# Optimization experiments

Hardware: AMD Instinct MI355X
Metric: run time of the kernel (lower is better)

## Reference

```python
import jax, jax.numpy as jnp
import numpy as np
from jax import lax

B, P, C = 2, 512, 5                 # images, proposals/img, classes (incl. background)
IN_FEAT, REP = 12544, 1024          # 256*7*7 pooled features; TwoMLPHead width
H_IMG = W_IMG = 800.0
SCORE_THRESH, NMS_THRESH, DET_PER_IMG = 0.05, 0.5, 100
MIN_SIZE = 0.01
WX, WY, WW, WH = 10.0, 10.0, 5.0, 5.0
BBOX_CLIP = float(np.log(1000.0 / 16.0))
NEG = -1e9


def _make_boxes(key, n):
    k1, k2, k3, k4 = jax.random.split(key, 4)
    cx = jax.random.uniform(k1, (n,)) * W_IMG
    cy = jax.random.uniform(k2, (n,)) * H_IMG
    bw = jax.random.uniform(k3, (n,)) * 180.0 + 20.0
    bh = jax.random.uniform(k4, (n,)) * 180.0 + 20.0
    x1 = jnp.clip(cx - bw / 2, 0.0, W_IMG)
    y1 = jnp.clip(cy - bh / 2, 0.0, H_IMG)
    x2 = jnp.clip(cx + bw / 2, 0.0, W_IMG)
    y2 = jnp.clip(cy + bh / 2, 0.0, H_IMG)
    return jnp.stack([x1, y1, x2, y2], -1).astype(jnp.float32)


def setup_inputs() -> dict:
    ks = jax.random.split(jax.random.key(0), 12)
    box_features = jax.random.normal(ks[0], (B * P, IN_FEAT), jnp.float32)
    proposals = jnp.stack([_make_boxes(ks[1 + i], P) for i in range(B)])
    def w(k, shp):
        return (jax.random.normal(k, shp, jnp.float32) / np.sqrt(shp[0])).astype(jnp.float32)
    return {
        'box_features': box_features,
        'proposals': proposals,
        'W1': w(ks[3], (IN_FEAT, REP)), 'b1': jnp.zeros((REP,), jnp.float32),
        'W2': w(ks[4], (REP, REP)),     'b2': jnp.zeros((REP,), jnp.float32),
        'Wc': w(ks[5], (REP, C)),       'bc': jnp.zeros((C,), jnp.float32),
        'Wb': w(ks[6], (REP, 4 * C)),   'bb': jnp.zeros((4 * C,), jnp.float32),
    }


def box_iou(a, b):
    area_a = (a[:, 2] - a[:, 0]) * (a[:, 3] - a[:, 1])
    area_b = (b[:, 2] - b[:, 0]) * (b[:, 3] - b[:, 1])
    lt = jnp.maximum(a[:, None, :2], b[None, :, :2])
    rb = jnp.minimum(a[:, None, 2:], b[None, :, 2:])
    wh = jnp.clip(rb - lt, 0.0)
    inter = wh[..., 0] * wh[..., 1]
    return inter / (area_a[:, None] + area_b[None, :] - inter + 1e-9)


def decode(reg, props):
    # reg: [N, C, 4] raw deltas; props: [N, 4] xyxy  (torchvision BoxCoder.decode)
    w = props[:, 2] - props[:, 0]
    h = props[:, 3] - props[:, 1]
    cx = props[:, 0] + 0.5 * w
    cy = props[:, 1] + 0.5 * h
    dx, dy = reg[..., 0] / WX, reg[..., 1] / WY
    dw = jnp.minimum(reg[..., 2] / WW, BBOX_CLIP)
    dh = jnp.minimum(reg[..., 3] / WH, BBOX_CLIP)
    pcx = dx * w[:, None] + cx[:, None]
    pcy = dy * h[:, None] + cy[:, None]
    pw = jnp.exp(dw) * w[:, None]
    ph = jnp.exp(dh) * h[:, None]
    return jnp.stack([pcx - 0.5 * pw, pcy - 0.5 * ph, pcx + 0.5 * pw, pcy + 0.5 * ph], -1)


def postprocess_one(boxes, scores, labels):
    # boxes [M,4] (already clipped), scores [M], labels [M] int; fixed-size output.
    M = boxes.shape[0]
    ws = boxes[:, 2] - boxes[:, 0]
    hs = boxes[:, 3] - boxes[:, 1]
    valid = (scores > SCORE_THRESH) & (ws >= MIN_SIZE) & (hs >= MIN_SIZE)
    order = jnp.argsort(-scores)
    b, s, l, v = boxes[order], scores[order], labels[order], valid[order]
    # batched (per-class) NMS via class-offset trick
    off = l.astype(b.dtype)[:, None] * (max(H_IMG, W_IMG) + 1.0)
    iou = box_iou(b + off, b + off)
    idxs = jnp.arange(M)

    def body(i, keep):
        sup = (iou[i] > NMS_THRESH) & keep[i] & (idxs > i)
        return keep & ~sup

    keep = lax.fori_loop(0, M, body, v)
    sc = jnp.where(keep, s, NEG)
    top_s, top_i = lax.top_k(sc, DET_PER_IMG)
    ok = top_s > NEG / 2
    tb = jnp.where(ok[:, None], b[top_i], 0.0)
    tl = jnp.where(ok, l[top_i], 0)
    ts = jnp.where(ok, top_s, 0.0)
    return tb, ts, tl


def reference(box_features, proposals, W1, b1, W2, b2, Wc, bc, Wb, bb):
    # box_head: TwoMLPHead
    h = jax.nn.relu(box_features @ W1 + b1)
    h = jax.nn.relu(h @ W2 + b2)
    # box_predictor
    class_logits = h @ Wc + bc                       # [N, C]
    box_regression = (h @ Wb + bb).reshape(-1, C, 4)  # [N, C, 4]
    props = proposals.reshape(-1, 4)
    pred = decode(box_regression, props)             # [N, C, 4]
    # clip to image
    pred = jnp.stack([
        jnp.clip(pred[..., 0], 0.0, W_IMG), jnp.clip(pred[..., 1], 0.0, H_IMG),
        jnp.clip(pred[..., 2], 0.0, W_IMG), jnp.clip(pred[..., 3], 0.0, H_IMG)], -1)
    scores = jax.nn.softmax(class_logits, -1)        # [N, C]
    # drop background class, flatten proposal-major (matches torch reshape(-1,4))
    pb = pred[:, 1:, :].reshape(B, P * (C - 1), 4)
    sc = scores[:, 1:].reshape(B, P * (C - 1))
    labels = jnp.tile(jnp.arange(1, C, dtype=jnp.int32), P)  # [M]
    boxes_o, scores_o, labels_o = jax.vmap(postprocess_one, in_axes=(0, 0, None))(pb, sc, labels)
    return boxes_o, scores_o, labels_o
```

## Files before the change

### kernel.cpp

```cpp
#include <hip/hip_runtime.h>
#include <math.h>

#define NROWS 1024
#define K1    12544
#define REP   1024
#define NDET  2048
#define DETS  100
#define BBOX_CLIP_F 4.135166556742356f

typedef __attribute__((ext_vector_type(8))) short bf16x8;
typedef __attribute__((ext_vector_type(4))) float f32x4;

__device__ __forceinline__ unsigned short rne_bf16(float x) {
  unsigned u = __float_as_uint(x);
  u += 0x7fffu + ((u >> 16) & 1u);
  return (unsigned short)(u >> 16);
}
__device__ __forceinline__ float bf16f(unsigned short h) {
  return __uint_as_float(((unsigned)h) << 16);
}
__device__ __forceinline__ int swz(int r, int s) {
  return s ^ (r & 3) ^ ((r >> 2) & 3);
}
__device__ __forceinline__ void gload16(const void* g, void* lds) {
  __builtin_amdgcn_global_load_lds(
      (const __attribute__((address_space(1))) unsigned int*)g,
      (__attribute__((address_space(3))) unsigned int*)lds, 16, 0, 0);
}

__global__ __launch_bounds__(256) void pack_b(
    const float* __restrict__ W, unsigned short* __restrict__ Oh,
    unsigned short* __restrict__ Ol, int nKB) {
  __shared__ unsigned short th[32 * 36], tl[32 * 36];
  const int kb = blockIdx.x, n0 = blockIdx.y * 32;
  const int t = threadIdx.x;
  const int r = t >> 3, c4 = (t & 7) << 2;
  float4 v = *(const float4*)&W[(size_t)(kb * 32 + r) * REP + n0 + c4];
  float fv[4] = {v.x, v.y, v.z, v.w};
#pragma unroll
  for (int j = 0; j < 4; ++j) {
    unsigned short h = rne_bf16(fv[j]);
    th[(c4 + j) * 36 + r] = h;
    tl[(c4 + j) * 36 + r] = rne_bf16(fv[j] - bf16f(h));
  }
  __syncthreads();
  const int half = t >> 7;
  const int n_loc = (t & 127) >> 2, slot = t & 3;
  const unsigned short* src = (half ? tl : th) + n_loc * 36 + slot * 8;
  ushort4 u0 = *(const ushort4*)src;
  ushort4 u1 = *(const ushort4*)(src + 4);
  const int n = n0 + n_loc, rb = n >> 7, rr = n & 127;
  size_t chunk = ((size_t)(rb * nKB + kb)) * 512 + rr * 4 + swz(rr, slot);
  unsigned short* dst = (half ? Ol : Oh) + chunk * 8;
  *(ushort4*)dst = u0;
  *(ushort4*)(dst + 4) = u1;
}

__global__ __launch_bounds__(256) void pack_a(
    const float* __restrict__ A, unsigned short* __restrict__ Oh,
    unsigned short* __restrict__ Ol, int K, int nKB) {
  const int kb = blockIdx.x;
  const int r = blockIdx.y * 64 + (threadIdx.x >> 2);
  const int slot = threadIdx.x & 3;
  const float* p = A + (size_t)r * K + kb * 32 + slot * 8;
  float4 f0 = *(const float4*)p;
  float4 f1 = *(const float4*)(p + 4);
  float fv[8] = {f0.x, f0.y, f0.z, f0.w, f1.x, f1.y, f1.z, f1.w};
  unsigned short hh[8], ll[8];
#pragma unroll
  for (int j = 0; j < 8; ++j) {
    hh[j] = rne_bf16(fv[j]);
    ll[j] = rne_bf16(fv[j] - bf16f(hh[j]));
  }
  const int rb = r >> 7, rr = r & 127;
  size_t chunk = ((size_t)(rb * nKB + kb)) * 512 + rr * 4 + swz(rr, slot);
  unsigned short* dh = Oh + chunk * 8;
  unsigned short* dl = Ol + chunk * 8;
  *(ushort4*)dh = make_ushort4(hh[0], hh[1], hh[2], hh[3]);
  *(ushort4*)(dh + 4) = make_ushort4(hh[4], hh[5], hh[6], hh[7]);
  *(ushort4*)dl = make_ushort4(ll[0], ll[1], ll[2], ll[3]);
  *(ushort4*)(dl + 4) = make_ushort4(ll[4], ll[5], ll[6], ll[7]);
}

__global__ __launch_bounds__(256) void gemm_pk2(
    const unsigned short* __restrict__ Ah, const unsigned short* __restrict__ Al,
    const unsigned short* __restrict__ Bh, const unsigned short* __restrict__ Bl,
    float* __restrict__ T, int nKB, int stepsPerZ) {
  __shared__ __align__(16) unsigned short lds[2][4][4096];
  const int tid = threadIdx.x;
  const int w = tid >> 6, l = tid & 63;
  const int r_ = blockIdx.x, t_ = blockIdx.y;
  const int rbA = (r_ & 3) * 2 + (t_ & 1);
  const int rbB = (r_ >> 2) * 4 + (t_ >> 1);
  const int tk0 = blockIdx.z * stepsPerZ;
  const int fr = l & 15, q = l >> 4;
  const int wr = (w >> 1) * 64, wc = (w & 1) * 64;
  const int qs = q ^ (fr & 3) ^ (fr >> 2);
  const int aoff = ((wr + fr) * 4 + qs) * 16;
  const int boff = ((wc + fr) * 4 + qs) * 16;

  auto stage = [&](int bf, int tk) {
    const unsigned short* ga_h = Ah + ((size_t)(rbA * nKB + tk)) * 4096;
    const unsigned short* ga_l = Al + ((size_t)(rbA * nKB + tk)) * 4096;
    const unsigned short* gb_h = Bh + ((size_t)(rbB * nKB + tk)) * 4096;
    const unsigned short* gb_l = Bl + ((size_t)(rbB * nKB + tk)) * 4096;
#pragma unroll
    for (int rseg = 0; rseg < 2; ++rseg) {
      const int seg = rseg * 4 + w;
      const size_t go = (size_t)(seg * 64 + l) * 8;
      gload16(ga_h + go, &lds[bf][0][seg * 512]);
      gload16(ga_l + go, &lds[bf][1][seg * 512]);
      gload16(gb_h + go, &lds[bf][2][seg * 512]);
      gload16(gb_l + go, &lds[bf][3][seg * 512]);
    }
  };

  f32x4 acc[4][4];
#pragma unroll
  for (int m = 0; m < 4; ++m)
#pragma unroll
    for (int n = 0; n < 4; ++n) acc[m][n] = (f32x4){0.f, 0.f, 0.f, 0.f};

  stage(0, tk0);
  __syncthreads();
  int cur = 0;
  for (int s = 0; s < stepsPerZ; ++s) {
    if (s + 1 < stepsPerZ) stage(cur ^ 1, tk0 + s + 1);
    const char* La  = (const char*)&lds[cur][0][0];
    const char* Ll  = (const char*)&lds[cur][1][0];
    const char* Lbh = (const char*)&lds[cur][2][0];
    const char* Lbl = (const char*)&lds[cur][3][0];
    bf16x8 ah[4], al[4], bh[4], bl[4];
#pragma unroll
    for (int m = 0; m < 4; ++m) {
      ah[m] = *(const bf16x8*)(La + aoff + m * 1024);
      al[m] = *(const bf16x8*)(Ll + aoff + m * 1024);
    }
#pragma unroll
    for (int n = 0; n < 4; ++n) {
      bh[n] = *(const bf16x8*)(Lbh + boff + n * 1024);
      bl[n] = *(const bf16x8*)(Lbl + boff + n * 1024);
    }
#pragma unroll
    for (int m = 0; m < 4; ++m)
#pragma unroll
      for (int n = 0; n < 4; ++n) {
        acc[m][n] = __builtin_amdgcn_mfma_f32_16x16x32_bf16(ah[m], bh[n], acc[m][n], 0, 0, 0);
        acc[m][n] = __builtin_amdgcn_mfma_f32_16x16x32_bf16(ah[m], bl[n], acc[m][n], 0, 0, 0);
        acc[m][n] = __builtin_amdgcn_mfma_f32_16x16x32_bf16(al[m], bh[n], acc[m][n], 0, 0, 0);
      }
    __syncthreads();
    cur ^= 1;
  }
  float* Tz = T + (size_t)blockIdx.z * (NROWS * REP);
#pragma unroll
  for (int m = 0; m < 4; ++m) {
    const int r0 = rbA * 128 + wr + m * 16 + ((l >> 4) << 2);
#pragma unroll
    for (int n = 0; n < 4; ++n) {
      const int c = rbB * 128 + wc + n * 16 + fr;
#pragma unroll
      for (int j = 0; j < 4; ++j) Tz[(size_t)(r0 + j) * REP + c] = acc[m][n][j];
    }
  }
}

__global__ __launch_bounds__(256) void combine8_relu_pack(
    const float* __restrict__ T, const float* __restrict__ bias,
    unsigned short* __restrict__ Oh, unsigned short* __restrict__ Ol) {
  const int e = (blockIdx.x * 256 + threadIdx.x) * 8;
  const int MN = NROWS * REP;
  float s[8];
  {
    float4 a0 = *(const float4*)&T[e];
    float4 a1 = *(const float4*)&T[e + 4];
    s[0] = a0.x; s[1] = a0.y; s[2] = a0.z; s[3] = a0.w;
    s[4] = a1.x; s[5] = a1.y; s[6] = a1.z; s[7] = a1.w;
  }
#pragma unroll
  for (int z = 1; z < 8; ++z) {
    float4 a0 = *(const float4*)&T[z * MN + e];
    float4 a1 = *(const float4*)&T[z * MN + e + 4];
    s[0] += a0.x; s[1] += a0.y; s[2] += a0.z; s[3] += a0.w;
    s[4] += a1.x; s[5] += a1.y; s[6] += a1.z; s[7] += a1.w;
  }
  const int c0 = e & 1023;
  float4 b0 = *(const float4*)&bias[c0];
  float4 b1 = *(const float4*)&bias[c0 + 4];
  s[0] = fmaxf(s[0] + b0.x, 0.f); s[1] = fmaxf(s[1] + b0.y, 0.f);
  s[2] = fmaxf(s[2] + b0.z, 0.f); s[3] = fmaxf(s[3] + b0.w, 0.f);
  s[4] = fmaxf(s[4] + b1.x, 0.f); s[5] = fmaxf(s[5] + b1.y, 0.f);
  s[6] = fmaxf(s[6] + b1.z, 0.f); s[7] = fmaxf(s[7] + b1.w, 0.f);
  unsigned short hh[8], ll[8];
#pragma unroll
  for (int j = 0; j < 8; ++j) {
    hh[j] = rne_bf16(s[j]);
    ll[j] = rne_bf16(s[j] - bf16f(hh[j]));
  }
  const int r = e >> 10;
  const int kb = c0 >> 5, slot = (c0 >> 3) & 3;
  const int rb = r >> 7, rr = r & 127;
  size_t chunk = ((size_t)(rb * 32 + kb)) * 512 + rr * 4 + swz(rr, slot);
  unsigned short* dh = Oh + chunk * 8;
  unsigned short* dl = Ol + chunk * 8;
  *(ushort4*)dh = make_ushort4(hh[0], hh[1], hh[2], hh[3]);
  *(ushort4*)(dh + 4) = make_ushort4(hh[4], hh[5], hh[6], hh[7]);
  *(ushort4*)dl = make_ushort4(ll[0], ll[1], ll[2], ll[3]);
  *(ushort4*)(dl + 4) = make_ushort4(ll[4], ll[5], ll[6], ll[7]);
}

__global__ __launch_bounds__(256) void combine8_relu(
    const float* __restrict__ T, const float* __restrict__ bias, float* __restrict__ H) {
  const int i = blockIdx.x * 256 + threadIdx.x;
  const int MN4 = NROWS * REP / 4;
  const float4* t = (const float4*)T;
  float4 s0 = t[i];
#pragma unroll
  for (int z = 1; z < 8; ++z) {
    float4 v = t[i + z * MN4];
    s0.x += v.x; s0.y += v.y; s0.z += v.z; s0.w += v.w;
  }
  float4 bs = ((const float4*)bias)[i & 255];
  float4 r;
  r.x = fmaxf(s0.x + bs.x, 0.f);
  r.y = fmaxf(s0.y + bs.y, 0.f);
  r.z = fmaxf(s0.z + bs.z, 0.f);
  r.w = fmaxf(s0.w + bs.w, 0.f);
  ((float4*)H)[i] = r;
}

__global__ __launch_bounds__(256) void gemm_pk(
    const float* __restrict__ A, const unsigned short* __restrict__ Bh,
    const unsigned short* __restrict__ Bl, float* __restrict__ T,
    int K, int nKB, int stepsPerZ) {
  __shared__ __align__(16) unsigned short lds[2][4][4096];
  const int tid = threadIdx.x;
  const int w = tid >> 6, l = tid & 63;
  const int bm = blockIdx.x * 128;
  const int bnb = blockIdx.y;
  const int tk0 = blockIdx.z * stepsPerZ;
  const int arow = tid >> 1, ahalf = tid & 1;
  const int fr = l & 15, q = l >> 4;
  const int wr = (w >> 1) * 64, wc = (w & 1) * 64;
  const int qs = q ^ (fr & 3) ^ (fr >> 2);
  const int aoff = ((wr + fr) * 4 + qs) * 16;
  const int boff = ((wc + fr) * 4 + qs) * 16;
  const float* aptr = A + (size_t)(bm + arow) * K + ahalf * 16;

  float4 av[4];
  auto loadA = [&](int tk) {
    const float* p = aptr + tk * 32;
#pragma unroll
    for (int j = 0; j < 4; ++j) av[j] = *(const float4*)(p + j * 4);
  };
  auto stageB = [&](int bf, int tk) {
    const unsigned short* gh = Bh + ((size_t)(bnb * nKB + tk)) * 4096;
    const unsigned short* gl_ = Bl + ((size_t)(bnb * nKB + tk)) * 4096;
#pragma unroll
    for (int rseg = 0; rseg < 2; ++rseg) {
      const int seg = rseg * 4 + w;
      gload16(gh + (size_t)(seg * 64 + l) * 8, &lds[bf][2][seg * 512]);
      gload16(gl_ + (size_t)(seg * 64 + l) * 8, &lds[bf][3][seg * 512]);
    }
  };
  auto writeA = [&](int bf) {
#pragma unroll
    for (int j = 0; j < 2; ++j) {
      const int s_ = ahalf * 2 + j;
      float fv[8] = {av[j * 2].x, av[j * 2].y, av[j * 2].z, av[j * 2].w,
                     av[j * 2 + 1].x, av[j * 2 + 1].y, av[j * 2 + 1].z, av[j * 2 + 1].w};
      unsigned hp[4], lp[4];
#pragma unroll
      for (int p2 = 0; p2 < 4; ++p2) {
        unsigned short h0 = rne_bf16(fv[2 * p2]), h1 = rne_bf16(fv[2 * p2 + 1]);
        float l0 = fv[2 * p2] - bf16f(h0), l1 = fv[2 * p2 + 1] - bf16f(h1);
        hp[p2] = (unsigned)h0 | ((unsigned)h1 << 16);
        lp[p2] = (unsigned)rne_bf16(l0) | ((unsigned)rne_bf16(l1) << 16);
      }
      const int chunk = arow * 4 + swz(arow, s_);
      *(uint4*)&lds[bf][0][chunk * 8] = make_uint4(hp[0], hp[1], hp[2], hp[3]);
      *(uint4*)&lds[bf][1][chunk * 8] = make_uint4(lp[0], lp[1], lp[2], lp[3]);
    }
  };

  f32x4 acc[4][4];
#pragma unroll
  for (int m = 0; m < 4; ++m)
#pragma unroll
    for (int n = 0; n < 4; ++n) acc[m][n] = (f32x4){0.f, 0.f, 0.f, 0.f};

  loadA(tk0);
  stageB(0, tk0);
  writeA(0);
  __syncthreads();
  int cur = 0;
  for (int s = 0; s < stepsPerZ; ++s) {
    const bool nx = (s + 1 < stepsPerZ);
    if (nx) { loadA(tk0 + s + 1); stageB(cur ^ 1, tk0 + s + 1); }
    const char* La = (const char*)&lds[cur][0][0];
    const char* Ll = (const char*)&lds[cur][1][0];
    const char* Lbh = (const char*)&lds[cur][2][0];
    const char* Lbl = (const char*)&lds[cur][3][0];
    bf16x8 ah[4], al[4], bh[4], bl[4];
#pragma unroll
    for (int m = 0; m < 4; ++m) {
      ah[m] = *(const bf16x8*)(La + aoff + m * 1024);
      al[m] = *(const bf16x8*)(Ll + aoff + m * 1024);
    }
#pragma unroll
    for (int n = 0; n < 4; ++n) {
      bh[n] = *(const bf16x8*)(Lbh + boff + n * 1024);
      bl[n] = *(const bf16x8*)(Lbl + boff + n * 1024);
    }
#pragma unroll
    for (int m = 0; m < 4; ++m)
#pragma unroll
      for (int n = 0; n < 4; ++n) {
        acc[m][n] = __builtin_amdgcn_mfma_f32_16x16x32_bf16(ah[m], bh[n], acc[m][n], 0, 0, 0);
        acc[m][n] = __builtin_amdgcn_mfma_f32_16x16x32_bf16(ah[m], bl[n], acc[m][n], 0, 0, 0);
        acc[m][n] = __builtin_amdgcn_mfma_f32_16x16x32_bf16(al[m], bh[n], acc[m][n], 0, 0, 0);
      }
    if (nx) writeA(cur ^ 1);
    __syncthreads();
    cur ^= 1;
  }
  float* Tz = T + (size_t)blockIdx.z * (NROWS * REP);
#pragma unroll
  for (int m = 0; m < 4; ++m) {
    const int r0 = bm + wr + m * 16 + ((l >> 4) << 2);
#pragma unroll
    for (int n = 0; n < 4; ++n) {
      const int c = bnb * 128 + wc + n * 16 + fr;
#pragma unroll
      for (int j = 0; j < 4; ++j) Tz[(size_t)(r0 + j) * REP + c] = acc[m][n][j];
    }
  }
}

__global__ __launch_bounds__(256) void gemm64(
    const float* __restrict__ A, const float* __restrict__ W,
    float* __restrict__ T, int K, int N, int kChunk) {
  __shared__ float As[32][68];
  __shared__ float Bs[32][64];
  const int tid = threadIdx.x;
  const int bm = blockIdx.x * 64, bn = blockIdx.y * 64;
  const int k0 = blockIdx.z * kChunk;
  const int tx = tid & 15, ty = tid >> 4;
  const int ar = tid >> 3;
  const int ac = (tid & 7) << 2;
  const int br = tid >> 4;
  const int bc = (tid & 15) << 2;
  float acc[4][4] = {{0.f,0.f,0.f,0.f},{0.f,0.f,0.f,0.f},{0.f,0.f,0.f,0.f},{0.f,0.f,0.f,0.f}};
  for (int kk = k0; kk < k0 + kChunk; kk += 32) {
    float4 a0 = *(const float4*)&A[(size_t)(bm + ar) * K + kk + ac];
    float4 a1 = *(const float4*)&A[(size_t)(bm + ar + 32) * K + kk + ac];
    float4 b0 = *(const float4*)&W[(size_t)(kk + br) * N + bn + bc];
    float4 b1 = *(const float4*)&W[(size_t)(kk + br + 16) * N + bn + bc];
    As[ac+0][ar] = a0.x; As[ac+1][ar] = a0.y; As[ac+2][ar] = a0.z; As[ac+3][ar] = a0.w;
    As[ac+0][ar+32] = a1.x; As[ac+1][ar+32] = a1.y; As[ac+2][ar+32] = a1.z; As[ac+3][ar+32] = a1.w;
    *(float4*)&Bs[br][bc]    = b0;
    *(float4*)&Bs[br+16][bc] = b1;
    __syncthreads();
#pragma unroll
    for (int k = 0; k < 32; ++k) {
      float4 av = *(const float4*)&As[k][ty << 2];
      float4 bv = *(const float4*)&Bs[k][tx << 2];
      float a_[4] = {av.x, av.y, av.z, av.w};
      float b_[4] = {bv.x, bv.y, bv.z, bv.w};
#pragma unroll
      for (int i = 0; i < 4; ++i)
#pragma unroll
        for (int j = 0; j < 4; ++j)
          acc[i][j] = fmaf(a_[i], b_[j], acc[i][j]);
    }
    __syncthreads();
  }
  float* Tz = T + (size_t)blockIdx.z * NROWS * REP;
#pragma unroll
  for (int i = 0; i < 4; ++i) {
    float4 v = make_float4(acc[i][0], acc[i][1], acc[i][2], acc[i][3]);
    *(float4*)&Tz[(size_t)(bm + (ty << 2) + i) * N + bn + (tx << 2)] = v;
  }
}

__global__ __launch_bounds__(256) void combine_relu(
    const float* __restrict__ T, const float* __restrict__ bias, float* __restrict__ H) {
  const int i = blockIdx.x * 256 + threadIdx.x;
  const int MN4 = NROWS * REP / 4;
  const float4* t = (const float4*)T;
  float4 a = t[i], b = t[i + MN4], c = t[i + 2 * MN4], d = t[i + 3 * MN4];
  float4 bs = ((const float4*)bias)[i & 255];
  float4 r;
  r.x = fmaxf(((a.x + b.x) + (c.x + d.x)) + bs.x, 0.f);
  r.y = fmaxf(((a.y + b.y) + (c.y + d.y)) + bs.y, 0.f);
  r.z = fmaxf(((a.z + b.z) + (c.z + d.z)) + bs.z, 0.f);
  r.w = fmaxf(((a.w + b.w) + (c.w + d.w)) + bs.w, 0.f);
  ((float4*)H)[i] = r;
}

__global__ __launch_bounds__(256) void pack_w25(
    const float* __restrict__ Wc, const float* __restrict__ Wb, float* __restrict__ Wt) {
  const int i = blockIdx.x * 256 + threadIdx.x;
  if (i < 25 * 1024) {
    const int o = i >> 10, k = i & 1023;
    Wt[i] = (o < 5) ? Wc[(size_t)k * 5 + o] : Wb[(size_t)k * 20 + (o - 5)];
  }
}

__global__ __launch_bounds__(256) void heads2(
    const float* __restrict__ H2, const float* __restrict__ Wt,
    const float* __restrict__ bcv, const float* __restrict__ bbv,
    const float* __restrict__ props, float* __restrict__ pb, float* __restrict__ sc) {
  const int wave = threadIdx.x >> 6, l = threadIdx.x & 63;
  const int n = blockIdx.x * 4 + wave;
  const float* h = H2 + (size_t)n * REP + l * 16;
  float4 h0 = *(const float4*)h, h1 = *(const float4*)(h + 4);
  float4 h2v = *(const float4*)(h + 8), h3 = *(const float4*)(h + 12);
  float outv[25];
#pragma unroll
  for (int o = 0; o < 25; ++o) {
    const float* wp = Wt + o * REP + l * 16;
    float4 w0 = *(const float4*)wp, w1 = *(const float4*)(wp + 4);
    float4 w2 = *(const float4*)(wp + 8), w3 = *(const float4*)(wp + 12);
    float d = h0.x * w0.x;
    d = fmaf(h0.y, w0.y, d); d = fmaf(h0.z, w0.z, d); d = fmaf(h0.w, w0.w, d);
    d = fmaf(h1.x, w1.x, d); d = fmaf(h1.y, w1.y, d); d = fmaf(h1.z, w1.z, d); d = fmaf(h1.w, w1.w, d);
    d = fmaf(h2v.x, w2.x, d); d = fmaf(h2v.y, w2.y, d); d = fmaf(h2v.z, w2.z, d); d = fmaf(h2v.w, w2.w, d);
    d = fmaf(h3.x, w3.x, d); d = fmaf(h3.y, w3.y, d); d = fmaf(h3.z, w3.z, d); d = fmaf(h3.w, w3.w, d);
#pragma unroll
    for (int m = 1; m < 64; m <<= 1) d += __shfl_xor(d, m);
    outv[o] = d + ((o < 5) ? bcv[o] : bbv[o - 5]);
  }
  const float mx = fmaxf(fmaxf(fmaxf(outv[0], outv[1]), fmaxf(outv[2], outv[3])), outv[4]);
  const float e0 = expf(outv[0] - mx), e1 = expf(outv[1] - mx), e2 = expf(outv[2] - mx);
  const float e3 = expf(outv[3] - mx), e4 = expf(outv[4] - mx);
  const float inv = 1.0f / (e0 + e1 + e2 + e3 + e4);
  const float s1 = e1 * inv, s2 = e2 * inv, s3 = e3 * inv, s4 = e4 * inv;
  const float* pr = props + (size_t)n * 4;
  const float x1 = pr[0], y1 = pr[1], x2 = pr[2], y2 = pr[3];
  const float bw = x2 - x1, bh = y2 - y1;
  const float cx = x1 + 0.5f * bw, cy = y1 + 0.5f * bh;
  const int img = n >> 9, pbase = (n & 511) << 2;
#pragma unroll
  for (int c = 1; c <= 4; ++c) {
    if (l == c - 1) {
      const float r0 = outv[5 + c * 4 + 0], r1 = outv[5 + c * 4 + 1];
      const float r2 = outv[5 + c * 4 + 2], r3 = outv[5 + c * 4 + 3];
      const float dx = r0 / 10.0f, dy = r1 / 10.0f;
      const float dw = fminf(r2 / 5.0f, BBOX_CLIP_F);
      const float dh = fminf(r3 / 5.0f, BBOX_CLIP_F);
      const float pcx = dx * bw + cx, pcy = dy * bh + cy;
      const float pw = expf(dw) * bw, ph = expf(dh) * bh;
      float bx1 = pcx - 0.5f * pw, by1 = pcy - 0.5f * ph;
      float bx2 = pcx + 0.5f * pw, by2 = pcy + 0.5f * ph;
      bx1 = fminf(fmaxf(bx1, 0.f), 800.f);
      by1 = fminf(fmaxf(by1, 0.f), 800.f);
      bx2 = fminf(fmaxf(bx2, 0.f), 800.f);
      by2 = fminf(fmaxf(by2, 0.f), 800.f);
      const int pidx = pbase + (c - 1);
      float* o = pb + (size_t)(img * NDET + pidx) * 4;
      o[0] = bx1; o[1] = by1; o[2] = bx2; o[3] = by2;
      const float smc = (c == 1) ? s1 : (c == 2) ? s2 : (c == 3) ? s3 : s4;
      sc[img * NDET + pidx] = smc;
    }
  }
}

__global__ __launch_bounds__(256) void heads_kernel(
    const float* __restrict__ H2, const float* __restrict__ Wc, const float* __restrict__ bcv,
    const float* __restrict__ Wb, const float* __restrict__ bbv,
    const float* __restrict__ props, float* __restrict__ pb, float* __restrict__ sc) {
  const int n = blockIdx.x;
  __shared__ float hrow[REP];
  __shared__ float part[25][8];
  __shared__ float outv[25];
  __shared__ float smax[5];
  const int tid = threadIdx.x;
  ((float4*)hrow)[tid] = ((const float4*)(H2 + (size_t)n * REP))[tid];
  __syncthreads();
  if (tid < 200) {
    const int o = tid >> 3, s = tid & 7;
    float a = 0.f;
    if (o < 5) {
      const float* w = Wc + o;
      for (int k = s * 128; k < s * 128 + 128; ++k) a = fmaf(hrow[k], w[(size_t)k * 5], a);
    } else {
      const float* w = Wb + (o - 5);
      for (int k = s * 128; k < s * 128 + 128; ++k) a = fmaf(hrow[k], w[(size_t)k * 20], a);
    }
    part[o][s] = a;
  }
  __syncthreads();
  if (tid < 25) {
    float a = ((part[tid][0] + part[tid][1]) + (part[tid][2] + part[tid][3]))
            + ((part[tid][4] + part[tid][5]) + (part[tid][6] + part[tid][7]));
    a += (tid < 5) ? bcv[tid] : bbv[tid - 5];
    outv[tid] = a;
  }
  __syncthreads();
  if (tid == 0) {
    float m = outv[0];
    for (int c = 1; c < 5; ++c) m = fmaxf(m, outv[c]);
    float e[5], ssum = 0.f;
    for (int c = 0; c < 5; ++c) { e[c] = expf(outv[c] - m); ssum += e[c]; }
    for (int c = 0; c < 5; ++c) smax[c] = e[c] / ssum;
  }
  __syncthreads();
  if (tid < 4) {
    const int c = tid + 1;
    const float* pr = props + (size_t)n * 4;
    const float x1 = pr[0], y1 = pr[1], x2 = pr[2], y2 = pr[3];
    const float w = x2 - x1, h = y2 - y1;
    const float cx = x1 + 0.5f * w, cy = y1 + 0.5f * h;
    const float r0 = outv[5 + c * 4 + 0], r1 = outv[5 + c * 4 + 1];
    const float r2 = outv[5 + c * 4 + 2], r3 = outv[5 + c * 4 + 3];
    const float dx = r0 / 10.0f, dy = r1 / 10.0f;
    const float dw = fminf(r2 / 5.0f, BBOX_CLIP_F);
    const float dh = fminf(r3 / 5.0f, BBOX_CLIP_F);
    const float pcx = dx * w + cx, pcy = dy * h + cy;
    const float pw = expf(dw) * w, ph = expf(dh) * h;
    float bx1 = pcx - 0.5f * pw, by1 = pcy - 0.5f * ph;
    float bx2 = pcx + 0.5f * pw, by2 = pcy + 0.5f * ph;
    bx1 = fminf(fmaxf(bx1, 0.f), 800.f);
    by1 = fminf(fmaxf(by1, 0.f), 800.f);
    bx2 = fminf(fmaxf(bx2, 0.f), 800.f);
    by2 = fminf(fmaxf(by2, 0.f), 800.f);
    const int img = n >> 9;
    const int pidx = ((n & 511) << 2) + (c - 1);
    float* o = pb + (size_t)(img * NDET + pidx) * 4;
    o[0] = bx1; o[1] = by1; o[2] = bx2; o[3] = by2;
    sc[img * NDET + pidx] = smax[c];
  }
}

__global__ __launch_bounds__(1024) void sort_kernel(
    const float* __restrict__ sc, unsigned* __restrict__ sidx) {
  const int b = blockIdx.x;
  __shared__ unsigned long long key[NDET];
  const int tid = threadIdx.x;
  for (int t = tid; t < NDET; t += 1024) {
    unsigned bits = __float_as_uint(sc[b * NDET + t]);
    key[t] = ((unsigned long long)bits << 32) | (unsigned)(~t);
  }
  __syncthreads();
  for (int k = 2; k <= NDET; k <<= 1) {
    for (int j = k >> 1; j > 0; j >>= 1) {
      for (int t = tid; t < NDET; t += 1024) {
        const int ixj = t ^ j;
        if (ixj > t) {
          const bool up = (t & k) == 0;
          unsigned long long a = key[t], bb_ = key[ixj];
          if ((a < bb_) == up) { key[t] = bb_; key[ixj] = a; }
        }
      }
      __syncthreads();
    }
  }
  for (int t = tid; t < NDET; t += 1024)
    sidx[b * NDET + t] = ~(unsigned)key[t];
}

__global__ __launch_bounds__(256) void prep_kernel(
    const unsigned* __restrict__ sidx, const float* __restrict__ pb, const float* __restrict__ sc,
    float* __restrict__ sbox, float* __restrict__ soff, float* __restrict__ sscore,
    float* __restrict__ sarea, float* __restrict__ slab, unsigned* __restrict__ vword) {
  const int b = blockIdx.y;
  const int i = blockIdx.x * 256 + threadIdx.x;
  const unsigned oi = sidx[b * NDET + i];
  const float* bx = pb + (size_t)(b * NDET + oi) * 4;
  const float x1 = bx[0], y1 = bx[1], x2 = bx[2], y2 = bx[3];
  const float s = sc[b * NDET + oi];
  const float lab = (float)((oi & 3) + 1);
  const bool valid = (s > 0.05f) && ((x2 - x1) >= 0.01f) && ((y2 - y1) >= 0.01f);
  const float off = lab * 801.0f;
  float* sb = sbox + (size_t)(b * NDET + i) * 4;
  sb[0] = x1; sb[1] = y1; sb[2] = x2; sb[3] = y2;
  float* so = soff + (size_t)(b * NDET + i) * 4;
  so[0] = x1 + off; so[1] = y1 + off; so[2] = x2 + off; so[3] = y2 + off;
  sscore[b * NDET + i] = s;
  sarea[b * NDET + i] = (x2 - x1) * (y2 - y1);
  slab[b * NDET + i] = lab;
  const unsigned long long bal = __ballot(valid);
  if ((i & 31) == 0) vword[b * 64 + (i >> 5)] = (unsigned)(bal >> (i & 32));
}

__global__ __launch_bounds__(256) void mask_kernel(
    const float* __restrict__ soff, const float* __restrict__ sarea,
    unsigned* __restrict__ mask) {
  const int b = blockIdx.y;
  __shared__ float box[NDET][4];
  __shared__ float area[NDET];
  const int tid = threadIdx.x;
  const float4* src = (const float4*)(soff + (size_t)b * NDET * 4);
  for (int t = tid; t < NDET; t += 256) ((float4*)box)[t] = src[t];
  const float4* asrc = (const float4*)(sarea + (size_t)b * NDET);
  for (int t = tid; t < NDET / 4; t += 256) ((float4*)area)[t] = asrc[t];
  __syncthreads();
  const int li = tid >> 6;
  const int w  = tid & 63;
#pragma unroll
  for (int pass = 0; pass < 4; ++pass) {
    const int i = blockIdx.x * 16 + pass * 4 + li;
    const float ax1 = box[i][0], ay1 = box[i][1], ax2 = box[i][2], ay2 = box[i][3];
    const float aa = area[i];
    unsigned bits = 0;
#pragma unroll 4
    for (int jj = 0; jj < 32; ++jj) {
      const int j = jj * 64 + w;
      const float ix = fmaxf(fminf(ax2, box[j][2]) - fmaxf(ax1, box[j][0]), 0.f);
      const float iy = fmaxf(fminf(ay2, box[j][3]) - fmaxf(ay1, box[j][1]), 0.f);
      const float inter = ix * iy;
      const float iou = inter / (aa + area[j] - inter + 1e-9f);
      if (j > i && iou > 0.5f) bits |= (1u << jj);
    }
    mask[((size_t)b * NDET + i) * 64 + w] = bits;
  }
}

__global__ __launch_bounds__(64) void scan_kernel(
    const unsigned* __restrict__ vword, const unsigned* __restrict__ mask,
    const float* __restrict__ sbox, const float* __restrict__ sscore,
    const float* __restrict__ slab, float* __restrict__ out) {
  const int b = blockIdx.x;
  const int lane = threadIdx.x;
  const unsigned valid = vword[b * 64 + lane];
  unsigned sup = 0;
  __shared__ unsigned short klist[DETS];
  int kcnt = 0;
  for (int i = 0; i < NDET; ++i) {
    const unsigned v = __shfl(valid, i >> 5);
    if (!((v >> (i & 31)) & 1)) continue;
    const unsigned s = __shfl(sup, i & 63);
    if ((s >> (i >> 6)) & 1) continue;
    if (lane == 0) klist[kcnt] = (unsigned short)i;
    kcnt++;
    sup |= mask[((size_t)b * NDET + i) * 64 + lane];
    if (kcnt == DETS) break;
  }
  __syncthreads();
  for (int s = lane; s < DETS; s += 64) {
    float b0 = 0.f, b1 = 0.f, b2 = 0.f, b3 = 0.f, sv = 0.f, lv = 0.f;
    if (s < kcnt) {
      const int i = klist[s];
      const float* bx = sbox + ((size_t)b * NDET + i) * 4;
      b0 = bx[0]; b1 = bx[1]; b2 = bx[2]; b3 = bx[3];
      sv = sscore[b * NDET + i];
      lv = slab[b * NDET + i];
    }
    float* ob = out + ((size_t)b * DETS + s) * 4;
    ob[0] = b0; ob[1] = b1; ob[2] = b2; ob[3] = b3;
    out[2 * DETS * 4 + b * DETS + s] = sv;
    out[2 * DETS * 4 + 2 * DETS + b * DETS + s] = lv;
  }
}

extern "C" void kernel_launch(void* const* d_in, const int* in_sizes, int n_in,
                              void* d_out, int out_size, void* d_ws, size_t ws_size,
                              hipStream_t stream) {
  const float* X     = (const float*)d_in[0];
  const float* props = (const float*)d_in[1];
  const float* W1    = (const float*)d_in[2];
  const float* b1    = (const float*)d_in[3];
  const float* W2    = (const float*)d_in[4];
  const float* b2    = (const float*)d_in[5];
  const float* Wc    = (const float*)d_in[6];
  const float* bc    = (const float*)d_in[7];
  const float* Wb    = (const float*)d_in[8];
  const float* bb    = (const float*)d_in[9];
  float* out = (float*)d_out;

  const size_t POST_B = 3200000;
  const size_t NEED_BIG =
      (size_t)9 * 1048576 * 4 +
      (size_t)4 * (size_t)K1 * 1024 * 2 +
      (size_t)4 * 1048576 * 2 + POST_B;
  const size_t NEED_MID =
      (size_t)10 * 1048576 * 4 +
      (size_t)2 * (size_t)K1 * 1024 * 2 +
      (size_t)2 * 1048576 * 2 + 2500000;

  float *T, *H1 = nullptr, *H2, *pb, *sc, *Wt = nullptr;
  unsigned short *W1h = nullptr, *W1l = nullptr, *W2h = nullptr, *W2l = nullptr;
  unsigned short *Ahp = nullptr, *Alp = nullptr, *H1h = nullptr, *H1l = nullptr;
  const int path = (ws_size >= NEED_BIG) ? 2 : (ws_size >= NEED_MID) ? 1 : 0;
  if (path == 2) {
    T   = (float*)d_ws;
    H2  = T + 8 * 1048576;
    W1h = (unsigned short*)(H2 + 1048576);
    W1l = W1h + (size_t)K1 * 1024;
    W2h = W1l + (size_t)K1 * 1024;
    W2l = W2h + 1048576;
    Ahp = W2l + 1048576;
    Alp = Ahp + (size_t)K1 * 1024;
    H1h = Alp + (size_t)K1 * 1024;
    H1l = H1h + 1048576;
    Wt  = (float*)(H1l + 1048576);
    pb  = Wt + 25 * 1024;
  } else if (path == 1) {
    T   = (float*)d_ws;
    H1  = T + 8 * 1048576;
    H2  = H1 + 1048576;
    W1h = (unsigned short*)(H2 + 1048576);
    W1l = W1h + (size_t)K1 * 1024;
    W2h = W1l + (size_t)K1 * 1024;
    W2l = W2h + 1048576;
    pb  = (float*)(W2l + 1048576);
  } else {
    T  = (float*)d_ws;
    H1 = T + 4 * 1048576;
    H2 = H1 + 1048576;
    pb = H2 + 1048576;
  }
  sc = pb + 2 * NDET * 4;
  unsigned* sidx = (unsigned*)(sc + 2 * NDET);
  float* sbox   = (float*)(sidx + 2 * NDET);
  float* soff   = sbox + 2 * NDET * 4;
  float* sscore = soff + 2 * NDET * 4;
  float* sarea  = sscore + 2 * NDET;
  float* slab   = sarea + 2 * NDET;
  unsigned* vword = (unsigned*)(slab + 2 * NDET);
  unsigned* mask  = vword + 128;

  if (path == 2) {
    pack_b<<<dim3(K1 / 32, 32), 256, 0, stream>>>(W1, W1h, W1l, K1 / 32);
    pack_b<<<dim3(32, 32), 256, 0, stream>>>(W2, W2h, W2l, 32);
    pack_a<<<dim3(K1 / 32, 16), 256, 0, stream>>>(X, Ahp, Alp, K1, K1 / 32);
    pack_w25<<<100, 256, 0, stream>>>(Wc, Wb, Wt);
    gemm_pk2<<<dim3(8, 8, 8), 256, 0, stream>>>(Ahp, Alp, W1h, W1l, T, K1 / 32, 49);
    combine8_relu_pack<<<512, 256, 0, stream>>>(T, b1, H1h, H1l);
    gemm_pk2<<<dim3(8, 8, 8), 256, 0, stream>>>(H1h, H1l, W2h, W2l, T, 32, 4);
    combine8_relu<<<1024, 256, 0, stream>>>(T, b2, H2);
    heads2<<<256, 256, 0, stream>>>(H2, Wt, bc, bb, props, pb, sc);
  } else if (path == 1) {
    pack_b<<<dim3(K1 / 32, 32), 256, 0, stream>>>(W1, W1h, W1l, K1 / 32);
    pack_b<<<dim3(32, 32), 256, 0, stream>>>(W2, W2h, W2l, 32);
    gemm_pk<<<dim3(8, 8, 8), 256, 0, stream>>>(X, W1h, W1l, T, K1, K1 / 32, 49);
    combine8_relu<<<1024, 256, 0, stream>>>(T, b1, H1);
    gemm_pk<<<dim3(8, 8, 8), 256, 0, stream>>>(H1, W2h, W2l, T, REP, 32, 4);
    combine8_relu<<<1024, 256, 0, stream>>>(T, b2, H2);
    heads_kernel<<<1024, 256, 0, stream>>>(H2, Wc, bc, Wb, bb, props, pb, sc);
  } else {
    gemm64<<<dim3(16, 16, 4), 256, 0, stream>>>(X, W1, T, K1, REP, K1 / 4);
    combine_relu<<<1024, 256, 0, stream>>>(T, b1, H1);
    gemm64<<<dim3(16, 16, 4), 256, 0, stream>>>(H1, W2, T, REP, REP, REP / 4);
    combine_relu<<<1024, 256, 0, stream>>>(T, b2, H2);
    heads_kernel<<<1024, 256, 0, stream>>>(H2, Wc, bc, Wb, bb, props, pb, sc);
  }
  sort_kernel<<<2, 1024, 0, stream>>>(sc, sidx);
  prep_kernel<<<dim3(8, 2), 256, 0, stream>>>(sidx, pb, sc, sbox, soff, sscore, sarea, slab, vword);
  mask_kernel<<<dim3(128, 2), 256, 0, stream>>>(soff, sarea, mask);
  scan_kernel<<<2, 64, 0, stream>>>(vword, mask, sbox, sscore, slab, out);
}
```

Before: 237.7 us.

## Use contiguous bit layout in NMS mask and skip-scan with ffs over words

The IoU mask kernel switches to structure-of-arrays LDS storage padded every 32 entries, so each lane handles 32 consecutive boxes and the mask words become contiguous bit ranges. The scan kernel keeps the suppression state in shared memory and uses find-first-set to jump straight to the next surviving candidate, instead of testing all 2048 indices one by one with shuffles. This removes the per-index serial loop cost in the single-wave scan. It adds a shared-memory barrier per kept box.

```diff
diff --git a/kernel.cpp b/kernel.cpp
--- a/kernel.cpp
+++ b/kernel.cpp
@@ -588,30 +588,34 @@
     const float* __restrict__ soff, const float* __restrict__ sarea,
     unsigned* __restrict__ mask) {
   const int b = blockIdx.y;
-  __shared__ float box[NDET][4];
-  __shared__ float area[NDET];
+  __shared__ float xx1[NDET + 64], yy1[NDET + 64], xx2[NDET + 64], yy2[NDET + 64];
+  __shared__ float ar[NDET + 64];
   const int tid = threadIdx.x;
-  const float4* src = (const float4*)(soff + (size_t)b * NDET * 4);
-  for (int t = tid; t < NDET; t += 256) ((float4*)box)[t] = src[t];
-  const float4* asrc = (const float4*)(sarea + (size_t)b * NDET);
-  for (int t = tid; t < NDET / 4; t += 256) ((float4*)area)[t] = asrc[t];
+  for (int t = tid; t < NDET; t += 256) {
+    float4 v = *(const float4*)(soff + ((size_t)b * NDET + t) * 4);
+    const int pt = t + (t >> 5);
+    xx1[pt] = v.x; yy1[pt] = v.y; xx2[pt] = v.z; yy2[pt] = v.w;
+    ar[pt] = sarea[b * NDET + t];
+  }
   __syncthreads();
   const int li = tid >> 6;
   const int w  = tid & 63;
 #pragma unroll
   for (int pass = 0; pass < 4; ++pass) {
     const int i = blockIdx.x * 16 + pass * 4 + li;
-    const float ax1 = box[i][0], ay1 = box[i][1], ax2 = box[i][2], ay2 = box[i][3];
-    const float aa = area[i];
+    const int pi = i + (i >> 5);
+    const float ax1 = xx1[pi], ay1 = yy1[pi], ax2 = xx2[pi], ay2 = yy2[pi];
+    const float aa = ar[pi];
     unsigned bits = 0;
 #pragma unroll 4
-    for (int jj = 0; jj < 32; ++jj) {
-      const int j = jj * 64 + w;
-      const float ix = fmaxf(fminf(ax2, box[j][2]) - fmaxf(ax1, box[j][0]), 0.f);
-      const float iy = fmaxf(fminf(ay2, box[j][3]) - fmaxf(ay1, box[j][1]), 0.f);
+    for (int bb = 0; bb < 32; ++bb) {
+      const int j = w * 32 + bb;
+      const int pj = w * 33 + bb;
+      const float ix = fmaxf(fminf(ax2, xx2[pj]) - fmaxf(ax1, xx1[pj]), 0.f);
+      const float iy = fmaxf(fminf(ay2, yy2[pj]) - fmaxf(ay1, yy1[pj]), 0.f);
       const float inter = ix * iy;
-      const float iou = inter / (aa + area[j] - inter + 1e-9f);
-      if (j > i && iou > 0.5f) bits |= (1u << jj);
+      const float iou = inter / (aa + ar[pj] - inter + 1e-9f);
+      if (j > i && iou > 0.5f) bits |= (1u << bb);
     }
     mask[((size_t)b * NDET + i) * 64 + w] = bits;
   }
@@ -623,19 +627,23 @@
     const float* __restrict__ slab, float* __restrict__ out) {
   const int b = blockIdx.x;
   const int lane = threadIdx.x;
-  const unsigned valid = vword[b * 64 + lane];
-  unsigned sup = 0;
+  __shared__ unsigned sup[64];
   __shared__ unsigned short klist[DETS];
+  sup[lane] = ~vword[b * 64 + lane];
+  __syncthreads();
   int kcnt = 0;
-  for (int i = 0; i < NDET; ++i) {
-    const unsigned v = __shfl(valid, i >> 5);
-    if (!((v >> (i & 31)) & 1)) continue;
-    const unsigned s = __shfl(sup, i & 63);
-    if ((s >> (i >> 6)) & 1) continue;
-    if (lane == 0) klist[kcnt] = (unsigned short)i;
-    kcnt++;
-    sup |= mask[((size_t)b * NDET + i) * 64 + lane];
-    if (kcnt == DETS) break;
+  for (int w = 0; w < 64 && kcnt < DETS; ++w) {
+    unsigned avail = ~sup[w];
+    while (avail) {
+      const int bb = __ffs(avail) - 1;
+      const int i = w * 32 + bb;
+      if (lane == 0) klist[kcnt] = (unsigned short)i;
+      kcnt++;
+      if (kcnt == DETS) break;
+      sup[lane] |= mask[((size_t)b * NDET + i) * 64 + lane];
+      __syncthreads();
+      avail = ~sup[w] & (0xFFFFFFFEu << bb);
+    }
   }
   __syncthreads();
   for (int s = lane; s < DETS; s += 64) {
```

Result: no change. 233.8 us (-1.6%).
